# Optimization experiments

Measured on AMD Instinct MI355X. Metric: run time of the kernel, lower is better.

## Reference

```python
import jax, jax.numpy as jnp
import numpy as np

N_NODES = 50000
N_EDGES = 800000
D_FEAT = 128
D_EMB = 128


def _spmm(row, col, val, x, n):
    # y[i] = sum_{e: row[e]==i} val[e] * x[col[e]]  -- COO spmm via gather + segment_sum
    return jax.ops.segment_sum(val[:, None] * x[col], row, num_segments=n)


def setup_inputs() -> dict:
    key = jax.random.key(0)
    k1, k2, k3, k4, k5 = jax.random.split(key, 5)
    feature = jax.random.normal(k1, (N_NODES, D_FEAT), dtype=jnp.float32)
    adj_row = jax.random.randint(k2, (N_EDGES,), 0, N_NODES, dtype=jnp.int32)
    adj_col = jax.random.randint(k3, (N_EDGES,), 0, N_NODES, dtype=jnp.int32)
    adj_val = jax.random.uniform(k4, (N_EDGES,), dtype=jnp.float32)
    stdv = 1.0 / np.sqrt(D_EMB)
    weight = jax.random.uniform(k5, (D_FEAT, D_EMB), minval=-stdv, maxval=stdv, dtype=jnp.float32)
    return {"feature": feature, "adj_row": adj_row, "adj_col": adj_col,
            "adj_val": adj_val, "weight": weight}


def reference(feature, adj_row, adj_col, adj_val, weight):
    n = feature.shape[0]
    h = _spmm(adj_row, adj_col, adj_val, feature, n)   # adj @ feature
    h = _spmm(adj_row, adj_col, adj_val, h, n)         # adj @ (adj @ feature)
    out = 0.5 * h - 0.5 * feature                      # elementwise combine
    return out @ weight                                # dense projection [N, D_EMB]
```

## Files before the change

kernel.cpp:

```cpp
#include <hip/hip_runtime.h>
#include <hip/hip_fp16.h>

#define D 128
#define CAP 48
#define NBMAX 128
#define BSHIFT 9
#define CB 9216
#define EPB 4096

typedef _Float16 f16;
typedef f16 f16x8 __attribute__((ext_vector_type(8)));
typedef float f32x4 __attribute__((ext_vector_type(4)));


__global__ __launch_bounds__(256) void conv_p1_kernel(
    const float* __restrict__ x, __half* __restrict__ xh,
    const float* __restrict__ W, __half* __restrict__ Wt,
    const int* __restrict__ row, const int* __restrict__ col,
    const float* __restrict__ val, int* __restrict__ bcur,
    int2* __restrict__ staging, long n8, int E, int nchunks) {
  if ((int)blockIdx.x >= nchunks) {
    long i = (long)((int)blockIdx.x - nchunks) * 256 + threadIdx.x;
    if (i < n8) {
      const float4* src = reinterpret_cast<const float4*>(x) + i * 2;
      float4 a = src[0], b = src[1];
      __half2 h0 = __floats2half2_rn(a.x, a.y);
      __half2 h1 = __floats2half2_rn(a.z, a.w);
      __half2 h2 = __floats2half2_rn(b.x, b.y);
      __half2 h3 = __floats2half2_rn(b.z, b.w);
      uint4 st;
      st.x = *reinterpret_cast<uint*>(&h0);
      st.y = *reinterpret_cast<uint*>(&h1);
      st.z = *reinterpret_cast<uint*>(&h2);
      st.w = *reinterpret_cast<uint*>(&h3);
      *(reinterpret_cast<uint4*>(xh) + i) = st;
    }
    if (i < D * D) {
      int k = (int)(i >> 7), j = (int)(i & 127);
      Wt[((long)j << 7) + k] = __float2half_rn(W[i]);
    }
    return;
  }
  __shared__ int bcnt[NBMAX];
  __shared__ int bbase[NBMAX];
  const int t = threadIdx.x;
  for (int b = t; b < NBMAX; b += 256) bcnt[b] = 0;
  __syncthreads();
  const int e0 = (int)blockIdx.x * EPB;
#pragma unroll
  for (int j = 0; j < EPB / 256; ++j) {
    int i = e0 + j * 256 + t;
    if (i < E) atomicAdd(&bcnt[row[i] >> BSHIFT], 1);
  }
  __syncthreads();
  for (int b = t; b < NBMAX; b += 256) {
    int c = bcnt[b];
    bbase[b] = (c > 0) ? atomicAdd(&bcur[b], c) : 0;
    bcnt[b] = 0;
  }
  __syncthreads();
#pragma unroll
  for (int j = 0; j < EPB / 256; ++j) {
    int i = e0 + j * 256 + t;
    if (i < E) {
      int r = row[i];
      int b = r >> BSHIFT;
      int p = atomicAdd(&bcnt[b], 1) + bbase[b];
      if (p < CB)
        staging[(long)b * CB + p] =
            make_int2(((r & 511) << 16) | col[i], __float_as_int(val[i]));
    }
  }
}


__global__ __launch_bounds__(256) void p2_kernel(
    const int* __restrict__ bcur, const int2* __restrict__ staging,
    int* __restrict__ cnt, int2* __restrict__ csrB, int N) {
  const int b = blockIdx.x;
  const int rlo = b << BSHIFT;
  __shared__ int rc[512];
  const int t = threadIdx.x;
  for (int j = t; j < 512; j += 256) rc[j] = 0;
  __syncthreads();
  const int cntE = min(bcur[b], CB);
  for (int i = t; i < cntE; i += 256) {
    int2 e = staging[(long)b * CB + i];
    int rloc = e.x >> 16;
    int c = e.x & 0xFFFF;
    int p = atomicAdd(&rc[rloc], 1);
    if (p < CAP) csrB[(long)(rlo + rloc) * CAP + p] = make_int2(c, e.y);
  }
  __syncthreads();
  for (int j = t; j < 512; j += 256) {
    int r = rlo + j;
    if (r < N) cnt[r] = rc[j];
  }
}


__device__ __forceinline__ float2 row_accum_wave(const int2* __restrict__ cv,
                                                 long s, long e,
                                                 const __half* __restrict__ xh,
                                                 int lane) {
  float2 acc = {0.f, 0.f};
  const int loff = lane << 1;
  long k = s;
  const long e8 = s + ((e - s) & ~7L);
  for (; k < e8; k += 8) {
    int2 c0 = cv[k + 0], c1 = cv[k + 1], c2 = cv[k + 2], c3 = cv[k + 3];
    int2 c4 = cv[k + 4], c5 = cv[k + 5], c6 = cv[k + 6], c7 = cv[k + 7];
    uint u0 = *reinterpret_cast<const uint*>(xh + ((long)c0.x << 7) + loff);
    uint u1 = *reinterpret_cast<const uint*>(xh + ((long)c1.x << 7) + loff);
    uint u2 = *reinterpret_cast<const uint*>(xh + ((long)c2.x << 7) + loff);
    uint u3 = *reinterpret_cast<const uint*>(xh + ((long)c3.x << 7) + loff);
    uint u4 = *reinterpret_cast<const uint*>(xh + ((long)c4.x << 7) + loff);
    uint u5 = *reinterpret_cast<const uint*>(xh + ((long)c5.x << 7) + loff);
    uint u6 = *reinterpret_cast<const uint*>(xh + ((long)c6.x << 7) + loff);
    uint u7 = *reinterpret_cast<const uint*>(xh + ((long)c7.x << 7) + loff);
#define ACC1(uu, cc)                                            \
    {                                                           \
      __half2 h = *reinterpret_cast<__half2*>(&(uu));           \
      float2 f = __half22float2(h);                             \
      float v = __int_as_float((cc).y);                         \
      acc.x = fmaf(v, f.x, acc.x);                              \
      acc.y = fmaf(v, f.y, acc.y);                              \
    }
    ACC1(u0, c0) ACC1(u1, c1) ACC1(u2, c2) ACC1(u3, c3)
    ACC1(u4, c4) ACC1(u5, c5) ACC1(u6, c6) ACC1(u7, c7)
  }
  for (; k < e; ++k) {
    int2 c = cv[k];
    uint u = *reinterpret_cast<const uint*>(xh + ((long)c.x << 7) + loff);
    ACC1(u, c)
  }
#undef ACC1
  return acc;
}


__global__ __launch_bounds__(256) void spmm1_kernel(
    const int* __restrict__ cnt, const int2* __restrict__ csrB,
    const __half* __restrict__ xh, __half* __restrict__ y, int N) {
  int r = blockIdx.x * 4 + (threadIdx.x >> 6);
  int lane = threadIdx.x & 63;
  if (r >= N) return;
  int deg = __builtin_amdgcn_readfirstlane(min(cnt[r], CAP));
  long s = (long)r * CAP;
  float2 acc = row_accum_wave(csrB, s, s + deg, xh, lane);
  __half2 p = __floats2half2_rn(acc.x, acc.y);
  *reinterpret_cast<__half2*>(y + ((long)r << 7) + (lane << 1)) = p;
}


__global__ __launch_bounds__(256) void spmm2z_kernel(
    const int* __restrict__ cnt, const int2* __restrict__ csrB,
    const __half* __restrict__ h1, const float* __restrict__ feat,
    __half* __restrict__ zh, int N) {
  int r = blockIdx.x * 4 + (threadIdx.x >> 6);
  int lane = threadIdx.x & 63;
  if (r >= N) return;
  int deg = __builtin_amdgcn_readfirstlane(min(cnt[r], CAP));
  long s = (long)r * CAP;
  float2 acc = row_accum_wave(csrB, s, s + deg, h1, lane);
  float2 fv = *reinterpret_cast<const float2*>(feat + ((long)r << 7) + (lane << 1));
  __half2 p = __floats2half2_rn(0.5f * (acc.x - fv.x), 0.5f * (acc.y - fv.y));
  *reinterpret_cast<__half2*>(zh + ((long)r << 7) + (lane << 1)) = p;
}


__global__ __launch_bounds__(256) void gemmz_mfma_kernel(
    const __half* __restrict__ zh, const __half* __restrict__ Wt,
    float* __restrict__ out, int N) {
  const int w = threadIdx.x >> 6;
  const int l = threadIdx.x & 63;
  const int r0 = blockIdx.x * 64 + w * 16;
  const int lr = l & 15;
  const int lk = (l >> 4) * 8;

  f16x8 a[4];
  const f16* zp = reinterpret_cast<const f16*>(zh) + ((long)(r0 + lr) << 7) + lk;
#pragma unroll
  for (int ks = 0; ks < 4; ++ks)
    a[ks] = *reinterpret_cast<const f16x8*>(zp + ks * 32);

  const int orow = r0 + (l >> 4) * 4;
#pragma unroll
  for (int jt = 0; jt < 8; ++jt) {
    const f16* wp = reinterpret_cast<const f16*>(Wt) + ((long)(jt * 16 + lr) << 7) + lk;
    f16x8 b0 = *reinterpret_cast<const f16x8*>(wp + 0);
    f16x8 b1 = *reinterpret_cast<const f16x8*>(wp + 32);
    f16x8 b2 = *reinterpret_cast<const f16x8*>(wp + 64);
    f16x8 b3 = *reinterpret_cast<const f16x8*>(wp + 96);
    f32x4 acc = {0.f, 0.f, 0.f, 0.f};
    acc = __builtin_amdgcn_mfma_f32_16x16x32_f16(a[0], b0, acc, 0, 0, 0);
    acc = __builtin_amdgcn_mfma_f32_16x16x32_f16(a[1], b1, acc, 0, 0, 0);
    acc = __builtin_amdgcn_mfma_f32_16x16x32_f16(a[2], b2, acc, 0, 0, 0);
    acc = __builtin_amdgcn_mfma_f32_16x16x32_f16(a[3], b3, acc, 0, 0, 0);
#pragma unroll
    for (int i = 0; i < 4; ++i) {
      int r = orow + i;
      if (r < N) out[((long)r << 7) + jt * 16 + lr] = acc[i];
    }
  }
}


__global__ __launch_bounds__(256) void spmm_atomic_kernel(
    const int* __restrict__ row, const int* __restrict__ col,
    const float* __restrict__ val, const float* __restrict__ x,
    float* __restrict__ y, int E) {
  long idx = (long)blockIdx.x * blockDim.x + threadIdx.x;
  int e = (int)(idx >> 5);
  if (e >= E) return;
  int q = (int)(idx & 31);
  int r = row[e];
  int c = col[e];
  float v = val[e];
  const float4 xv = *reinterpret_cast<const float4*>(x + (long)c * D + q * 4);
  float* yp = y + (long)r * D + q * 4;
  atomicAdd(yp + 0, v * xv.x);
  atomicAdd(yp + 1, v * xv.y);
  atomicAdd(yp + 2, v * xv.z);
  atomicAdd(yp + 3, v * xv.w);
}

__global__ __launch_bounds__(256) void combine_gemm_kernel(
    const float* __restrict__ h2, const float* __restrict__ feat,
    const float* __restrict__ W, float* __restrict__ out, int N) {
  __shared__ float Xs[32][D];
  const int t = threadIdx.x;
  const int rb = blockIdx.x * 32;
#pragma unroll
  for (int i = 0; i < 4; ++i) {
    int o = i * 1024 + t * 4;
    int r = o >> 7;
    int cc = o & 127;
    float4 xv = {0.f, 0.f, 0.f, 0.f};
    if (rb + r < N) {
      float4 hv = *reinterpret_cast<const float4*>(h2 + (long)(rb + r) * D + cc);
      float4 fv = *reinterpret_cast<const float4*>(feat + (long)(rb + r) * D + cc);
      xv.x = 0.5f * (hv.x - fv.x);
      xv.y = 0.5f * (hv.y - fv.y);
      xv.z = 0.5f * (hv.z - fv.z);
      xv.w = 0.5f * (hv.w - fv.w);
    }
    *reinterpret_cast<float4*>(&Xs[r][cc]) = xv;
  }
  __syncthreads();
  const int j0 = (t & 31) * 4;
  const int i0 = (t >> 5) * 4;
  float4 acc[4];
#pragma unroll
  for (int ii = 0; ii < 4; ++ii) acc[ii] = {0.f, 0.f, 0.f, 0.f};
#pragma unroll 8
  for (int kb = 0; kb < 32; ++kb) {
    float4 xr[4], wr[4];
#pragma unroll
    for (int ii = 0; ii < 4; ++ii)
      xr[ii] = *reinterpret_cast<const float4*>(&Xs[i0 + ii][kb * 4]);
#pragma unroll
    for (int kk = 0; kk < 4; ++kk)
      wr[kk] = *reinterpret_cast<const float4*>(W + (kb * 4 + kk) * D + j0);
#pragma unroll
    for (int ii = 0; ii < 4; ++ii) {
      const float* xp = &xr[ii].x;
#pragma unroll
      for (int kk = 0; kk < 4; ++kk) {
        float xk = xp[kk];
        acc[ii].x = fmaf(xk, wr[kk].x, acc[ii].x);
        acc[ii].y = fmaf(xk, wr[kk].y, acc[ii].y);
        acc[ii].z = fmaf(xk, wr[kk].z, acc[ii].z);
        acc[ii].w = fmaf(xk, wr[kk].w, acc[ii].w);
      }
    }
  }
#pragma unroll
  for (int ii = 0; ii < 4; ++ii) {
    int r = rb + i0 + ii;
    if (r < N)
      *reinterpret_cast<float4*>(out + (long)r * D + j0) = acc[ii];
  }
}


static inline size_t align256(size_t x) { return (x + 255) & ~(size_t)255; }

extern "C" void kernel_launch(void* const* d_in, const int* in_sizes, int n_in,
                              void* d_out, int out_size, void* d_ws, size_t ws_size,
                              hipStream_t stream) {
  const float* feature = (const float*)d_in[0];
  const int* adj_row   = (const int*)d_in[1];
  const int* adj_col   = (const int*)d_in[2];
  const float* adj_val = (const float*)d_in[3];
  const float* weight  = (const float*)d_in[4];
  float* out = (float*)d_out;

  const int N = in_sizes[0] / D;
  const int E = in_sizes[1];
  const size_t hbytes  = (size_t)N * D * sizeof(float);
  const size_t hbytes2 = (size_t)N * D * sizeof(__half);
  const int nb = (N + 511) >> BSHIFT;

  char* p = (char*)d_ws;
  int* bcur      = (int*)p;    p += align256((size_t)NBMAX * 4);
  int* cnt       = (int*)p;    p += align256((size_t)N * 4);
  __half* wt     = (__half*)p; p += align256((size_t)D * D * 2);
  int2* csrB     = (int2*)p;   p += align256((size_t)N * CAP * 8);
  __half* feath  = (__half*)p; p += align256(hbytes2);
  const size_t need = (size_t)(p - (char*)d_ws);
  const size_t stage_need = hbytes2 + (size_t)nb * CB * 8;

  if (ws_size >= need && nb <= NBMAX && N < 65536 &&
      stage_need <= (size_t)out_size * 4) {
    __half* h1h = (__half*)d_out;
    int2* staging = (int2*)((char*)d_out + hbytes2);
    const long n8 = (long)N * D / 8;
    const int convB = (int)((n8 + 255) / 256);
    const int nchunks = (E + EPB - 1) / EPB;
    hipMemsetAsync(bcur, 0, (size_t)NBMAX * 4, stream);
    conv_p1_kernel<<<nchunks + convB, 256, 0, stream>>>(
        feature, feath, weight, wt, adj_row, adj_col, adj_val,
        bcur, staging, n8, E, nchunks);
    p2_kernel<<<nb, 256, 0, stream>>>(bcur, staging, cnt, csrB, N);
    spmm1_kernel<<<(N + 3) / 4, 256, 0, stream>>>(cnt, csrB, feath, h1h, N);
    spmm2z_kernel<<<(N + 3) / 4, 256, 0, stream>>>(cnt, csrB, h1h, feature,
                                                   feath, N);
    gemmz_mfma_kernel<<<(N + 63) / 64, 256, 0, stream>>>(feath, wt, out, N);
  } else {
    float* fh1 = out;
    float* fh2 = (float*)d_ws;
    const long items = (long)E * 32;
    const int spmm_blocks = (int)((items + 255) / 256);
    hipMemsetAsync(fh1, 0, hbytes, stream);
    spmm_atomic_kernel<<<spmm_blocks, 256, 0, stream>>>(adj_row, adj_col, adj_val,
                                                        feature, fh1, E);
    hipMemsetAsync(fh2, 0, hbytes, stream);
    spmm_atomic_kernel<<<spmm_blocks, 256, 0, stream>>>(adj_row, adj_col, adj_val,
                                                        fh1, fh2, E);
    combine_gemm_kernel<<<(N + 31) / 32, 256, 0, stream>>>(fh2, feature, weight,
                                                           out, N);
  }
}
```

Baseline: 147.3 us.

## Fuse second SpMM, combine and MFMA projection into one kernel

```diff
diff --git a/kernel.cpp b/kernel.cpp
--- a/kernel.cpp
+++ b/kernel.cpp
@@ -153,6 +153,56 @@
 }
 
 
+__global__ __launch_bounds__(256) void spmm2g_kernel(
+    const int* __restrict__ cnt, const int2* __restrict__ csrB,
+    const __half* __restrict__ h1, const float* __restrict__ feat,
+    const __half* __restrict__ Wt, float* __restrict__ out, int N) {
+  __shared__ __half zbuf[64][136];
+  const int w = threadIdx.x >> 6;
+  const int lane = threadIdx.x & 63;
+  const int rbase = blockIdx.x * 64 + w * 16;
+
+  for (int rr = 0; rr < 16; ++rr) {
+    int r = rbase + rr;
+    if (r < N) {
+      int deg = __builtin_amdgcn_readfirstlane(min(cnt[r], CAP));
+      long s = (long)r * CAP;
+      float2 acc = row_accum_wave(csrB, s, s + deg, h1, lane);
+      float2 fv = *reinterpret_cast<const float2*>(feat + ((long)r << 7) + (lane << 1));
+      __half2 p = __floats2half2_rn(0.5f * (acc.x - fv.x), 0.5f * (acc.y - fv.y));
+      *reinterpret_cast<__half2*>(&zbuf[w * 16 + rr][lane << 1]) = p;
+    }
+  }
+
+  const int lr = lane & 15;
+  const int lk = (lane >> 4) * 8;
+  f16x8 a[4];
+#pragma unroll
+  for (int ks = 0; ks < 4; ++ks)
+    a[ks] = *reinterpret_cast<const f16x8*>(&zbuf[w * 16 + lr][lk + ks * 32]);
+
+  const int orow = rbase + (lane >> 4) * 4;
+#pragma unroll
+  for (int jt = 0; jt < 8; ++jt) {
+    const f16* wp = reinterpret_cast<const f16*>(Wt) + ((long)(jt * 16 + lr) << 7) + lk;
+    f16x8 b0 = *reinterpret_cast<const f16x8*>(wp + 0);
+    f16x8 b1 = *reinterpret_cast<const f16x8*>(wp + 32);
+    f16x8 b2 = *reinterpret_cast<const f16x8*>(wp + 64);
+    f16x8 b3 = *reinterpret_cast<const f16x8*>(wp + 96);
+    f32x4 acc = {0.f, 0.f, 0.f, 0.f};
+    acc = __builtin_amdgcn_mfma_f32_16x16x32_f16(a[0], b0, acc, 0, 0, 0);
+    acc = __builtin_amdgcn_mfma_f32_16x16x32_f16(a[1], b1, acc, 0, 0, 0);
+    acc = __builtin_amdgcn_mfma_f32_16x16x32_f16(a[2], b2, acc, 0, 0, 0);
+    acc = __builtin_amdgcn_mfma_f32_16x16x32_f16(a[3], b3, acc, 0, 0, 0);
+#pragma unroll
+    for (int i = 0; i < 4; ++i) {
+      int r = orow + i;
+      if (r < N) out[((long)r << 7) + jt * 16 + lr] = acc[i];
+    }
+  }
+}
+
+
 __global__ __launch_bounds__(256) void spmm2z_kernel(
     const int* __restrict__ cnt, const int2* __restrict__ csrB,
     const __half* __restrict__ h1, const float* __restrict__ feat,
@@ -168,7 +218,6 @@
   *reinterpret_cast<__half2*>(zh + ((long)r << 7) + (lane << 1)) = p;
 }
 
-
 __global__ __launch_bounds__(256) void gemmz_mfma_kernel(
     const __half* __restrict__ zh, const __half* __restrict__ Wt,
     float* __restrict__ out, int N) {
@@ -177,13 +226,11 @@
   const int r0 = blockIdx.x * 64 + w * 16;
   const int lr = l & 15;
   const int lk = (l >> 4) * 8;
-
   f16x8 a[4];
   const f16* zp = reinterpret_cast<const f16*>(zh) + ((long)(r0 + lr) << 7) + lk;
 #pragma unroll
   for (int ks = 0; ks < 4; ++ks)
     a[ks] = *reinterpret_cast<const f16x8*>(zp + ks * 32);
-
   const int orow = r0 + (l >> 4) * 4;
 #pragma unroll
   for (int jt = 0; jt < 8; ++jt) {
@@ -307,27 +354,53 @@
   int* cnt       = (int*)p;    p += align256((size_t)N * 4);
   __half* wt     = (__half*)p; p += align256((size_t)D * D * 2);
   int2* csrB     = (int2*)p;   p += align256((size_t)N * CAP * 8);
+  int2* stagingW = (int2*)p;   p += align256((size_t)nb * CB * 8);
   __half* feath  = (__half*)p; p += align256(hbytes2);
-  const size_t need = (size_t)(p - (char*)d_ws);
+  __half* h1h    = (__half*)p; p += align256(hbytes2);
+  const size_t needA = (size_t)(p - (char*)d_ws);
+
+  const long n8 = (long)N * D / 8;
+  const int convB = (int)((n8 + 255) / 256);
+  const int nchunks = (E + EPB - 1) / EPB;
+
+  if (ws_size >= needA && nb <= NBMAX && N < 65536) {
+    hipMemsetAsync(bcur, 0, (size_t)NBMAX * 4, stream);
+    conv_p1_kernel<<<nchunks + convB, 256, 0, stream>>>(
+        feature, feath, weight, wt, adj_row, adj_col, adj_val,
+        bcur, stagingW, n8, E, nchunks);
+    p2_kernel<<<nb, 256, 0, stream>>>(bcur, stagingW, cnt, csrB, N);
+    spmm1_kernel<<<(N + 3) / 4, 256, 0, stream>>>(cnt, csrB, feath, h1h, N);
+    spmm2g_kernel<<<(N + 63) / 64, 256, 0, stream>>>(cnt, csrB, h1h, feature,
+                                                     wt, out, N);
+    return;
+  }
+
+  p = (char*)d_ws;
+  bcur      = (int*)p;    p += align256((size_t)NBMAX * 4);
+  cnt       = (int*)p;    p += align256((size_t)N * 4);
+  wt        = (__half*)p; p += align256((size_t)D * D * 2);
+  csrB      = (int2*)p;   p += align256((size_t)N * CAP * 8);
+  feath     = (__half*)p; p += align256(hbytes2);
+  const size_t needB = (size_t)(p - (char*)d_ws);
   const size_t stage_need = hbytes2 + (size_t)nb * CB * 8;
 
-  if (ws_size >= need && nb <= NBMAX && N < 65536 &&
+  if (ws_size >= needB && nb <= NBMAX && N < 65536 &&
       stage_need <= (size_t)out_size * 4) {
-    __half* h1h = (__half*)d_out;
+    __half* h1h_o = (__half*)d_out;
     int2* staging = (int2*)((char*)d_out + hbytes2);
-    const long n8 = (long)N * D / 8;
-    const int convB = (int)((n8 + 255) / 256);
-    const int nchunks = (E + EPB - 1) / EPB;
     hipMemsetAsync(bcur, 0, (size_t)NBMAX * 4, stream);
     conv_p1_kernel<<<nchunks + convB, 256, 0, stream>>>(
         feature, feath, weight, wt, adj_row, adj_col, adj_val,
         bcur, staging, n8, E, nchunks);
     p2_kernel<<<nb, 256, 0, stream>>>(bcur, staging, cnt, csrB, N);
-    spmm1_kernel<<<(N + 3) / 4, 256, 0, stream>>>(cnt, csrB, feath, h1h, N);
-    spmm2z_kernel<<<(N + 3) / 4, 256, 0, stream>>>(cnt, csrB, h1h, feature,
+    spmm1_kernel<<<(N + 3) / 4, 256, 0, stream>>>(cnt, csrB, feath, h1h_o, N);
+    spmm2z_kernel<<<(N + 3) / 4, 256, 0, stream>>>(cnt, csrB, h1h_o, feature,
                                                    feath, N);
     gemmz_mfma_kernel<<<(N + 63) / 64, 256, 0, stream>>>(feath, wt, out, N);
-  } else {
+    return;
+  }
+
+  {
     float* fh1 = out;
     float* fh2 = (float*)d_ws;
     const long items = (long)E * 32;
```

New measurement: 167.0 us. +13.4%, slower.
